# Kernel optimization log

Measured on AMD Instinct MI355X. Metric: run time of the kernel, lower is better.

The kernel has to match this reference:

```python
import jax, jax.numpy as jnp
import numpy as np

EMB, HID, V_SRC, V_TGT, NUM_OUT, BOS = 128, 512, 10000, 8000, 9, 0


def _lstm_cell(x, h, c, Wih, Whh, bih, bhh):
    # PyTorch LSTMCell math: gates ordered i, f, g, o
    g = x @ Wih.T + h @ Whh.T + (bih + bhh)
    i, f, gg, o = jnp.split(g, 4, axis=-1)
    i, f, o = jax.nn.sigmoid(i), jax.nn.sigmoid(f), jax.nn.sigmoid(o)
    c = f * c + i * jnp.tanh(gg)
    h = o * jnp.tanh(c)
    return h, c


def setup_inputs() -> dict:
    key = jax.random.key(0)
    ks = jax.random.split(key, 12)
    s = 1.0 / np.sqrt(HID)
    u = lambda k, shp: jax.random.uniform(k, shp, jnp.float32, -s, s)
    src = jax.random.randint(ks[0], (2048, 2), 0, V_SRC)
    src_embed = jax.random.normal(ks[1], (V_SRC, EMB), jnp.float32)
    src_embed = src_embed.at[0].set(0.0)  # padding_idx row
    tgt_embed = jax.random.normal(ks[2], (V_TGT, EMB), jnp.float32)
    tgt_embed = tgt_embed.at[BOS].set(0.0)  # padding_idx=BOS row
    return {
        "src": src,
        "src_embed": src_embed,
        "tgt_embed": tgt_embed,
        "enc_Wih": u(ks[3], (4 * HID, EMB)),
        "enc_Whh": u(ks[4], (4 * HID, HID)),
        "enc_bih": u(ks[5], (4 * HID,)),
        "enc_bhh": u(ks[6], (4 * HID,)),
        "dec_Wih": u(ks[7], (4 * HID, EMB)),
        "dec_Whh": u(ks[8], (4 * HID, HID)),
        "dec_bih": u(ks[9], (4 * HID,)),
        "dec_bhh": u(ks[10], (4 * HID,)),
        "proj_W": u(ks[11], (V_TGT, HID)),
        "proj_b": jnp.zeros((V_TGT,), jnp.float32),
    }


def reference(src, src_embed, tgt_embed, enc_Wih, enc_Whh, enc_bih, enc_bhh,
              dec_Wih, dec_Whh, dec_bih, dec_bhh, proj_W, proj_b):
    B = src.shape[0]
    # ---- encoder over the 2 source tokens ----
    enc_in = src_embed[src]  # (B, 2, EMB); dropout is identity at inference
    h = jnp.zeros((B, HID), jnp.float32)
    c = jnp.zeros((B, HID), jnp.float32)

    def enc_step(carry, x_t):
        h, c = carry
        h, c = _lstm_cell(x_t, h, c, enc_Wih, enc_Whh, enc_bih, enc_bhh)
        return (h, c), None

    (h, c), _ = jax.lax.scan(enc_step, (h, c), jnp.swapaxes(enc_in, 0, 1))

    token0 = jnp.full((B,), BOS, jnp.int32)

    def dec_step(carry, _):
        token, h, c = carry
        x = tgt_embed[token]  # (B, EMB)
        h, c = _lstm_cell(x, h, c, dec_Wih, dec_Whh, dec_bih, dec_bhh)
        logit = h @ proj_W.T + proj_b  # (B, V_TGT)
        nxt = jnp.argmax(logit, axis=-1).astype(jnp.int32)
        return (nxt, h, c), logit

    _, step_logits = jax.lax.scan(dec_step, (token0, h, c), None, length=NUM_OUT)
    # step_logits: (NUM_OUT, B, V_TGT) -> max-pool over steps
    return jnp.max(step_logits, axis=0)
```

## Files before the change

### kernel.cpp

```cpp
#include <hip/hip_runtime.h>
#include <math.h>

#define BB 2048
#define EMB 128
#define HID 512
#define G4 2048
#define VT 8000
#define VTP2 8192
#define NSTEP 9
#define NTILE2 64
#define LDW 132

typedef short bf16x8 __attribute__((ext_vector_type(8)));
typedef float f32x4 __attribute__((ext_vector_type(4)));

__device__ __forceinline__ ushort f2bf(float x) {
    uint u = __float_as_uint(x);
    uint r = (u + 0x7fffu + ((u >> 16) & 1u)) >> 16;
    return (ushort)r;
}
__device__ __forceinline__ float bf2f(ushort h) {
    return __uint_as_float(((uint)h) << 16);
}
__device__ __forceinline__ float sigm(float x) { return 1.0f / (1.0f + expf(-x)); }

__device__ __forceinline__ void gload16(const ushort* g, ushort* l) {
    __builtin_amdgcn_global_load_lds(
        (const __attribute__((address_space(1))) uint*)g,
        (__attribute__((address_space(3))) uint*)l, 16, 0, 0);
}

__device__ __forceinline__ void stage4(
    ushort* Sb,
    const ushort* __restrict__ Ah, const ushort* __restrict__ Al,
    const ushort* __restrict__ Bh, const ushort* __restrict__ Bl,
    int biA, int biB, int K, int k0, int wid, int lane)
{
    const ushort* src = (wid < 2) ? ((wid == 0) ? Ah : Al)
                                  : ((wid == 2) ? Bh : Bl);
    const int rowbase = (wid < 2) ? biA : biB;
    const int rl = lane >> 2, kcp = lane & 3;
    #pragma unroll
    for (int j = 0; j < 8; ++j) {
        int row = j * 16 + rl;
        int kc = (kcp - (row >> 1)) & 3;
        const ushort* g = src + (size_t)(rowbase + row) * K + k0 + kc * 8;
        gload16(g, Sb + wid * 4096 + j * 512);
    }
}

__device__ __forceinline__ void stage8(
    ushort* Sb,
    const ushort* __restrict__ Ah, const ushort* __restrict__ Al,
    const ushort* __restrict__ Bh, const ushort* __restrict__ Bl,
    int biA, int biB, int K, int k0, int wid, int lane)
{
    const int rl = lane >> 2, kcp = lane & 3;
    #pragma unroll
    for (int j = 0; j < 4; ++j) {
        int c = wid * 4 + j;
        int region = c >> 3;
        int rowblk = c & 7;
        int row = rowblk * 16 + rl;
        int kc = (kcp - (row >> 1)) & 3;
        const ushort* src = (region < 2) ? (region == 0 ? Ah : Al)
                                         : (region == 2 ? Bh : Bl);
        int base = (region < 2) ? biA : biB;
        gload16(src + (size_t)(base + row) * K + k0 + kc * 8,
                Sb + region * 4096 + rowblk * 512);
    }
}

__global__ __launch_bounds__(64) void gather2_kernel(
    ushort* __restrict__ Xhi, ushort* __restrict__ Xlo,
    const float* __restrict__ table,
    const int* __restrict__ src, int mode, int offset,
    const float* __restrict__ partval, const int* __restrict__ partidx)
{
    int row = blockIdx.x, t = threadIdx.x;
    int tok;
    if (mode == 0) {
        tok = src[row * 2 + offset];
    } else if (mode == 1) {
        tok = 0;
    } else {
        float v = partval[(size_t)row * NTILE2 + t];
        int  ix = partidx[(size_t)row * NTILE2 + t];
        #pragma unroll
        for (int off = 1; off < 64; off <<= 1) {
            float ov = __shfl_xor(v, off, 64);
            int   oi = __shfl_xor(ix, off, 64);
            if (ov > v || (ov == v && oi < ix)) { v = ov; ix = oi; }
        }
        tok = ix;
    }
    float2 e = *(const float2*)&table[(size_t)tok * EMB + t * 2];
    ushort2 hh, hl;
    hh.x = f2bf(e.x); hl.x = f2bf(e.x - bf2f(hh.x));
    hh.y = f2bf(e.y); hl.y = f2bf(e.y - bf2f(hh.y));
    *(ushort2*)&Xhi[row * EMB + t * 2] = hh;
    *(ushort2*)&Xlo[row * EMB + t * 2] = hl;
}

__global__ __launch_bounds__(256) void convgate_kernel(
    const float* __restrict__ W, ushort* __restrict__ Whi, ushort* __restrict__ Wlo,
    int kshift)
{
    size_t e0 = ((size_t)blockIdx.x * 256 + threadIdx.x) * 8;
    int K = 1 << kshift;
    int in_row = (int)(e0 >> kshift);
    int q = in_row & 511, gate = in_row >> 9;
    size_t o0 = (((size_t)(q * 4 + gate)) << kshift) + (e0 & (K - 1));
    float4 v0 = *(const float4*)&W[e0];
    float4 v1 = *(const float4*)&W[e0 + 4];
    float x[8] = {v0.x, v0.y, v0.z, v0.w, v1.x, v1.y, v1.z, v1.w};
    uint p[4], qq[4];
    #pragma unroll
    for (int j = 0; j < 4; ++j) {
        ushort h0 = f2bf(x[2 * j]),     l0 = f2bf(x[2 * j] - bf2f(h0));
        ushort h1 = f2bf(x[2 * j + 1]), l1 = f2bf(x[2 * j + 1] - bf2f(h1));
        p[j]  = (uint)h0 | ((uint)h1 << 16);
        qq[j] = (uint)l0 | ((uint)l1 << 16);
    }
    *(uint4*)&Whi[o0] = make_uint4(p[0], p[1], p[2], p[3]);
    *(uint4*)&Wlo[o0] = make_uint4(qq[0], qq[1], qq[2], qq[3]);
}

__global__ __launch_bounds__(256) void convgbias_kernel(
    const float* __restrict__ b0, const float* __restrict__ b1, float* __restrict__ bp)
{
    int i = blockIdx.x * 256 + threadIdx.x;
    int q = i >> 2, gate = i & 3;
    bp[i] = b0[gate * 512 + q] + b1[gate * 512 + q];
}

__global__ __launch_bounds__(256) void convw_kernel(
    const float* __restrict__ W, ushort* __restrict__ Whi, ushort* __restrict__ Wlo)
{
    size_t e0 = ((size_t)blockIdx.x * 256 + threadIdx.x) * 8;
    int row = (int)(e0 >> 9);
    uint p[4], q[4];
    if (row < VT) {
        float4 v0 = *(const float4*)&W[e0];
        float4 v1 = *(const float4*)&W[e0 + 4];
        float x[8] = {v0.x, v0.y, v0.z, v0.w, v1.x, v1.y, v1.z, v1.w};
        #pragma unroll
        for (int j = 0; j < 4; ++j) {
            ushort h0 = f2bf(x[2 * j]),     l0 = f2bf(x[2 * j] - bf2f(h0));
            ushort h1 = f2bf(x[2 * j + 1]), l1 = f2bf(x[2 * j + 1] - bf2f(h1));
            p[j] = (uint)h0 | ((uint)h1 << 16);
            q[j] = (uint)l0 | ((uint)l1 << 16);
        }
    } else {
        #pragma unroll
        for (int j = 0; j < 4; ++j) { p[j] = 0u; q[j] = 0u; }
    }
    *(uint4*)&Whi[e0] = make_uint4(p[0], p[1], p[2], p[3]);
    *(uint4*)&Wlo[e0] = make_uint4(q[0], q[1], q[2], q[3]);
}

__global__ __launch_bounds__(256) void convb_kernel(
    const float* __restrict__ b, float* __restrict__ bp)
{
    int i = blockIdx.x * 256 + threadIdx.x;
    if (i < VTP2) bp[i] = (i < VT) ? b[i] : -1e30f;
}

__global__ __launch_bounds__(512) void gatescell_kernel(
    const ushort* __restrict__ Xhi, const ushort* __restrict__ Xlo,
    const ushort* __restrict__ Hhi, const ushort* __restrict__ Hlo,
    const ushort* __restrict__ WihH, const ushort* __restrict__ WihL,
    const ushort* __restrict__ WhhH, const ushort* __restrict__ WhhL,
    const float* __restrict__ bperm,
    float* __restrict__ Cst,
    ushort* __restrict__ OHhi, ushort* __restrict__ OHlo,
    int nk)
{
    __shared__ __align__(16) char smem[128 * LDW * 4];
    ushort* S0 = (ushort*)smem;

    const int t = threadIdx.x;
    const int n = blockIdx.x;
    const int tile = (n & 7) * 2 + ((n >> 3) & 1);
    const int rb = n >> 4;
    const int bj0 = tile * 128;
    const int bi0 = rb * 128;
    const int il = t & 15;
    const int g  = (t >> 4) & 3;
    const int wid = t >> 6;
    const int lane = t & 63;
    const int wr = wid >> 2;
    const int wc = wid & 3;

    int aofs[4], bofs[2];
    #pragma unroll
    for (int m = 0; m < 4; ++m) {
        int r = wr * 64 + m * 16 + il;
        aofs[m] = r * 32 + (((g + (r >> 1)) & 3) << 3);
    }
    #pragma unroll
    for (int nn = 0; nn < 2; ++nn) {
        int r = wc * 32 + nn * 16 + il;
        bofs[nn] = 8192 + r * 32 + (((g + (r >> 1)) & 3) << 3);
    }

    f32x4 acc[4][2];
    #pragma unroll
    for (int m = 0; m < 4; ++m)
        #pragma unroll
        for (int nn = 0; nn < 2; ++nn) acc[m][nn] = 0.0f;

    stage8(S0, Xhi, Xlo, WihH, WihL, bi0, bj0, EMB, 0, wid, lane);

    for (int ks = 0; ks < nk; ++ks) {
        int cur = ks & 1;
        if (ks + 1 < nk) {
            int kn = ks + 1;
            if (kn < 4) stage8(S0 + (cur ^ 1) * 16384, Xhi, Xlo, WihH, WihL, bi0, bj0, EMB, kn * 32, wid, lane);
            else        stage8(S0 + (cur ^ 1) * 16384, Hhi, Hlo, WhhH, WhhL, bi0, bj0, HID, (kn - 4) * 32, wid, lane);
        }
        if (ks + 1 < nk) asm volatile("s_waitcnt vmcnt(4)" ::: "memory");
        else             asm volatile("s_waitcnt vmcnt(0)" ::: "memory");
        __builtin_amdgcn_s_barrier();
        __builtin_amdgcn_sched_barrier(0);

        ushort* Sb = S0 + cur * 16384;
        bf16x8 ah[4], al[4];
        #pragma unroll
        for (int m = 0; m < 4; ++m) {
            ah[m] = *(const bf16x8*)&Sb[aofs[m]];
            al[m] = *(const bf16x8*)&Sb[4096 + aofs[m]];
        }
        #pragma unroll
        for (int nn = 0; nn < 2; ++nn) {
            bf16x8 bh = *(const bf16x8*)&Sb[bofs[nn]];
            bf16x8 bl = *(const bf16x8*)&Sb[4096 + bofs[nn]];
            #pragma unroll
            for (int m = 0; m < 4; ++m) {
                acc[m][nn] = __builtin_amdgcn_mfma_f32_16x16x32_bf16(ah[m], bh, acc[m][nn], 0, 0, 0);
                acc[m][nn] = __builtin_amdgcn_mfma_f32_16x16x32_bf16(ah[m], bl, acc[m][nn], 0, 0, 0);
                acc[m][nn] = __builtin_amdgcn_mfma_f32_16x16x32_bf16(al[m], bh, acc[m][nn], 0, 0, 0);
            }
        }
        __builtin_amdgcn_sched_barrier(0);
        __builtin_amdgcn_s_barrier();
        __builtin_amdgcn_sched_barrier(0);
    }

    float* Tr = (float*)smem;
    float bn[2];
    #pragma unroll
    for (int nn = 0; nn < 2; ++nn) bn[nn] = bperm[bj0 + wc * 32 + nn * 16 + il];

    #pragma unroll
    for (int m = 0; m < 4; ++m)
        #pragma unroll
        for (int nn = 0; nn < 2; ++nn)
            #pragma unroll
            for (int j = 0; j < 4; ++j)
                Tr[(wr * 64 + m * 16 + g * 4 + j) * LDW + wc * 32 + nn * 16 + il]
                    = acc[m][nn][j] + bn[nn];
    __syncthreads();

    #pragma unroll
    for (int it = 0; it < 8; ++it) {
        int row = it * 16 + (t >> 5);
        int c4 = t & 31;
        float4 gv = *(float4*)&Tr[row * LDW + c4 * 4];
        float gi = sigm(gv.x), gf = sigm(gv.y), gg = tanhf(gv.z), go = sigm(gv.w);
        size_t o = (size_t)(bi0 + row) * HID + (bj0 >> 2) + c4;
        float cnew = gf * Cst[o] + gi * gg;
        float h = go * tanhf(cnew);
        Cst[o] = cnew;
        ushort hh = f2bf(h);
        OHhi[o] = hh;
        OHlo[o] = f2bf(h - bf2f(hh));
    }
}

__global__ __launch_bounds__(256) void proj_kernel(
    const ushort* __restrict__ Ahi, const ushort* __restrict__ Alo,
    const ushort* __restrict__ Whi, const ushort* __restrict__ Wlo,
    const float* __restrict__ biasp,
    float* __restrict__ outmax,
    float* __restrict__ partval, int* __restrict__ partidx,
    int mode)
{
    __shared__ __align__(16) char smem[128 * LDW * 4];
    ushort* S0 = (ushort*)smem;

    const int t = threadIdx.x;
    const int n = blockIdx.x;
    const int xcd = n & 7;
    const int j8 = n >> 3;
    const int tile = xcd * 8 + (j8 & 7);
    const int rb = j8 >> 3;
    const int bj0 = tile * 128;
    const int bi0 = rb * 128;
    const int il = t & 15;
    const int g  = (t >> 4) & 3;
    const int wid = t >> 6;
    const int lane = t & 63;
    const int wr = wid >> 1, wc = wid & 1;

    float4 oldv[16];
    const bool rmw = (mode == 2);
    if (rmw) {
        #pragma unroll
        for (int it = 0; it < 16; ++it) {
            int row2 = it * 8 + (t >> 5);
            oldv[it] = *(const float4*)&outmax[(size_t)(bi0 + row2) * VT + bj0 + (t & 31) * 4];
        }
    }

    int aofs[4], bofs[4];
    #pragma unroll
    for (int m = 0; m < 4; ++m) {
        int r = wr * 64 + m * 16 + il;
        aofs[m] = r * 32 + (((g + (r >> 1)) & 3) << 3);
    }
    #pragma unroll
    for (int nn = 0; nn < 4; ++nn) {
        int r = wc * 64 + nn * 16 + il;
        bofs[nn] = 8192 + r * 32 + (((g + (r >> 1)) & 3) << 3);
    }

    f32x4 acc[4][4];
    #pragma unroll
    for (int m = 0; m < 4; ++m)
        #pragma unroll
        for (int nn = 0; nn < 4; ++nn) acc[m][nn] = 0.0f;

    stage4(S0, Ahi, Alo, Whi, Wlo, bi0, bj0, HID, 0, wid, lane);

    for (int ks = 0; ks < 16; ++ks) {
        int cur = ks & 1;
        if (ks + 1 < 16)
            stage4(S0 + (cur ^ 1) * 16384, Ahi, Alo, Whi, Wlo, bi0, bj0, HID, (ks + 1) * 32, wid, lane);
        if (ks + 1 < 16) asm volatile("s_waitcnt vmcnt(8)" ::: "memory");
        else             asm volatile("s_waitcnt vmcnt(0)" ::: "memory");
        __builtin_amdgcn_s_barrier();
        __builtin_amdgcn_sched_barrier(0);

        ushort* Sb = S0 + cur * 16384;
        bf16x8 ah[4], al[4];
        #pragma unroll
        for (int m = 0; m < 4; ++m) {
            ah[m] = *(const bf16x8*)&Sb[aofs[m]];
            al[m] = *(const bf16x8*)&Sb[4096 + aofs[m]];
        }
        #pragma unroll
        for (int nn = 0; nn < 4; ++nn) {
            bf16x8 bh = *(const bf16x8*)&Sb[bofs[nn]];
            bf16x8 bl = *(const bf16x8*)&Sb[4096 + bofs[nn]];
            #pragma unroll
            for (int m = 0; m < 4; ++m) {
                acc[m][nn] = __builtin_amdgcn_mfma_f32_16x16x32_bf16(ah[m], bh, acc[m][nn], 0, 0, 0);
                acc[m][nn] = __builtin_amdgcn_mfma_f32_16x16x32_bf16(ah[m], bl, acc[m][nn], 0, 0, 0);
                acc[m][nn] = __builtin_amdgcn_mfma_f32_16x16x32_bf16(al[m], bh, acc[m][nn], 0, 0, 0);
            }
        }
        __builtin_amdgcn_sched_barrier(0);
        __builtin_amdgcn_s_barrier();
        __builtin_amdgcn_sched_barrier(0);
    }

    float* Tr = (float*)smem;
    float bn[4];
    #pragma unroll
    for (int nn = 0; nn < 4; ++nn) bn[nn] = biasp[bj0 + wc * 64 + nn * 16 + il];

    #pragma unroll
    for (int m = 0; m < 4; ++m)
        #pragma unroll
        for (int nn = 0; nn < 4; ++nn)
            #pragma unroll
            for (int j = 0; j < 4; ++j)
                Tr[(wr * 64 + m * 16 + g * 4 + j) * LDW + wc * 64 + nn * 16 + il]
                    = acc[m][nn][j] + bn[nn];
    __syncthreads();

    #pragma unroll
    for (int it = 0; it < 16; ++it) {
        int row2 = it * 8 + (t >> 5);
        int c4 = t & 31;
        int row = bi0 + row2;
        int col = bj0 + c4 * 4;
        float4 cur = *(float4*)&Tr[row2 * LDW + c4 * 4];

        float bv = cur.x; int bix = col;
        if (cur.y > bv) { bv = cur.y; bix = col + 1; }
        if (cur.z > bv) { bv = cur.z; bix = col + 2; }
        if (cur.w > bv) { bv = cur.w; bix = col + 3; }
        #pragma unroll
        for (int off = 1; off < 32; off <<= 1) {
            float ov = __shfl_xor(bv, off, 64);
            int   oi = __shfl_xor(bix, off, 64);
            if (ov > bv || (ov == bv && oi < bix)) { bv = ov; bix = oi; }
        }
        if ((t & 31) == 0) {
            partval[(size_t)row * NTILE2 + tile] = bv;
            partidx[(size_t)row * NTILE2 + tile] = bix;
        }

        if (col < VT) {
            float4 o = cur;
            if (rmw) {
                float4 p = oldv[it];
                o.x = fmaxf(o.x, p.x); o.y = fmaxf(o.y, p.y);
                o.z = fmaxf(o.z, p.z); o.w = fmaxf(o.w, p.w);
            }
            *(float4*)&outmax[(size_t)row * VT + col] = o;
        }
    }
}

extern "C" void kernel_launch(void* const* d_in, const int* in_sizes, int n_in,
                              void* d_out, int out_size, void* d_ws, size_t ws_size,
                              hipStream_t stream) {
    const int*   src       = (const int*)d_in[0];
    const float* src_embed = (const float*)d_in[1];
    const float* tgt_embed = (const float*)d_in[2];
    const float* enc_Wih   = (const float*)d_in[3];
    const float* enc_Whh   = (const float*)d_in[4];
    const float* enc_bih   = (const float*)d_in[5];
    const float* enc_bhh   = (const float*)d_in[6];
    const float* dec_Wih   = (const float*)d_in[7];
    const float* dec_Whh   = (const float*)d_in[8];
    const float* dec_bih   = (const float*)d_in[9];
    const float* dec_bhh   = (const float*)d_in[10];
    const float* proj_W    = (const float*)d_in[11];
    const float* proj_b    = (const float*)d_in[12];
    float* out = (float*)d_out;

    char* ws = (char*)d_ws;
    float*  C     = (float*)ws;   ws += (size_t)BB * HID * 4;
    float*  PV    = (float*)ws;   ws += (size_t)BB * NTILE2 * 4;
    int*    PI    = (int*)ws;     ws += (size_t)BB * NTILE2 * 4;
    ushort* Xhi   = (ushort*)ws;  ws += (size_t)BB * EMB * 2;
    ushort* Xlo   = (ushort*)ws;  ws += (size_t)BB * EMB * 2;
    ushort* Hhi   = (ushort*)ws;  ws += (size_t)BB * HID * 2;
    ushort* Hlo   = (ushort*)ws;  ws += (size_t)BB * HID * 2;
    ushort* PWhi  = (ushort*)ws;  ws += (size_t)VTP2 * HID * 2;
    ushort* PWlo  = (ushort*)ws;  ws += (size_t)VTP2 * HID * 2;
    float*  biasp = (float*)ws;   ws += (size_t)VTP2 * 4;
    ushort* eWihH = (ushort*)ws;  ws += (size_t)G4 * EMB * 2;
    ushort* eWihL = (ushort*)ws;  ws += (size_t)G4 * EMB * 2;
    ushort* eWhhH = (ushort*)ws;  ws += (size_t)G4 * HID * 2;
    ushort* eWhhL = (ushort*)ws;  ws += (size_t)G4 * HID * 2;
    ushort* dWihH = (ushort*)ws;  ws += (size_t)G4 * EMB * 2;
    ushort* dWihL = (ushort*)ws;  ws += (size_t)G4 * EMB * 2;
    ushort* dWhhH = (ushort*)ws;  ws += (size_t)G4 * HID * 2;
    ushort* dWhhL = (ushort*)ws;  ws += (size_t)G4 * HID * 2;
    float*  BSe   = (float*)ws;   ws += (size_t)G4 * 4;
    float*  BSd   = (float*)ws;   ws += (size_t)G4 * 4;

    hipMemsetAsync(C, 0, (size_t)BB * HID * 4, stream);

    convw_kernel<<<VTP2 * HID / 8 / 256, 256, 0, stream>>>(proj_W, PWhi, PWlo);
    convb_kernel<<<VTP2 / 256, 256, 0, stream>>>(proj_b, biasp);
    convgate_kernel<<<G4 * EMB / 8 / 256, 256, 0, stream>>>(enc_Wih, eWihH, eWihL, 7);
    convgate_kernel<<<G4 * HID / 8 / 256, 256, 0, stream>>>(enc_Whh, eWhhH, eWhhL, 9);
    convgate_kernel<<<G4 * EMB / 8 / 256, 256, 0, stream>>>(dec_Wih, dWihH, dWihL, 7);
    convgate_kernel<<<G4 * HID / 8 / 256, 256, 0, stream>>>(dec_Whh, dWhhH, dWhhL, 9);
    convgbias_kernel<<<G4 / 256, 256, 0, stream>>>(enc_bih, enc_bhh, BSe);
    convgbias_kernel<<<G4 / 256, 256, 0, stream>>>(dec_bih, dec_bhh, BSd);

    for (int tstep = 0; tstep < 2; ++tstep) {
        gather2_kernel<<<BB, 64, 0, stream>>>(Xhi, Xlo, src_embed, src, 0, tstep, PV, PI);
        gatescell_kernel<<<256, 512, 0, stream>>>(Xhi, Xlo, Hhi, Hlo,
            eWihH, eWihL, eWhhH, eWhhL, BSe, C, Hhi, Hlo, tstep == 0 ? 4 : 20);
    }

    for (int s = 0; s < NSTEP; ++s) {
        gather2_kernel<<<BB, 64, 0, stream>>>(Xhi, Xlo, tgt_embed, nullptr,
            (s == 0 ? 1 : 2), 0, PV, PI);
        gatescell_kernel<<<256, 512, 0, stream>>>(Xhi, Xlo, Hhi, Hlo,
            dWihH, dWihL, dWhhH, dWhhL, BSd, C, Hhi, Hlo, 20);
        proj_kernel<<<1024, 256, 0, stream>>>(Hhi, Hlo, PWhi, PWlo, biasp,
            out, PV, PI, (s == 0 ? 1 : 2));
    }
}
```

Measured before the change: 1.043 ms.

## Enlarge projection tiles to 128x256 with triple-buffered split-phase LDS pipeline

The projection GEMM moves from 128x128 tiles with 256 threads and double buffering to 128x256 tiles with 512 threads. It uses a three-stage LDS ring, and each k-step is split into two halves with interleaved loads and setprio around the MFMA blocks. The epilogue now writes the output and argmax per 16-row chunk through a smaller transpose buffer, reading the old max values inline instead of prefetching them into registers. The per-row partial argmax count drops from 64 to 32 tiles. The goal is more reuse of each staged tile and better overlap of loads with compute, at the cost of 144KB of LDS and one block per CU.

```diff
diff --git a/kernel.cpp b/kernel.cpp
--- a/kernel.cpp
+++ b/kernel.cpp
@@ -8,7 +8,7 @@
 #define VT 8000
 #define VTP2 8192
 #define NSTEP 9
-#define NTILE2 64
+#define PT 32
 #define LDW 132
 
 typedef short bf16x8 __attribute__((ext_vector_type(8)));
@@ -28,25 +28,6 @@
     __builtin_amdgcn_global_load_lds(
         (const __attribute__((address_space(1))) uint*)g,
         (__attribute__((address_space(3))) uint*)l, 16, 0, 0);
-}
-
-__device__ __forceinline__ void stage4(
-    ushort* Sb,
-    const ushort* __restrict__ Ah, const ushort* __restrict__ Al,
-    const ushort* __restrict__ Bh, const ushort* __restrict__ Bl,
-    int biA, int biB, int K, int k0, int wid, int lane)
-{
-    const ushort* src = (wid < 2) ? ((wid == 0) ? Ah : Al)
-                                  : ((wid == 2) ? Bh : Bl);
-    const int rowbase = (wid < 2) ? biA : biB;
-    const int rl = lane >> 2, kcp = lane & 3;
-    #pragma unroll
-    for (int j = 0; j < 8; ++j) {
-        int row = j * 16 + rl;
-        int kc = (kcp - (row >> 1)) & 3;
-        const ushort* g = src + (size_t)(rowbase + row) * K + k0 + kc * 8;
-        gload16(g, Sb + wid * 4096 + j * 512);
-    }
 }
 
 __device__ __forceinline__ void stage8(
@@ -71,6 +52,27 @@
     }
 }
 
+__device__ __forceinline__ void stage3h(
+    ushort* Sb,
+    const ushort* __restrict__ Ah, const ushort* __restrict__ Al,
+    const ushort* __restrict__ Bh, const ushort* __restrict__ Bl,
+    int biA, int biB, int k0, int wid, int lane, int half)
+{
+    const int rl = lane >> 2, kcp = lane & 3;
+    #pragma unroll
+    for (int j = 0; j < 3; ++j) {
+        int c = wid * 6 + half * 3 + j;
+        const ushort* src;
+        int row, base;
+        if (c < 8)       { src = Ah; row = c * 16 + rl;        base = biA; }
+        else if (c < 16) { src = Al; row = (c - 8) * 16 + rl;  base = biA; }
+        else if (c < 32) { src = Bh; row = (c - 16) * 16 + rl; base = biB; }
+        else             { src = Bl; row = (c - 32) * 16 + rl; base = biB; }
+        int kc = (kcp - (row >> 1)) & 3;
+        gload16(src + (size_t)(base + row) * HID + k0 + kc * 8, Sb + c * 512);
+    }
+}
+
 __global__ __launch_bounds__(64) void gather2_kernel(
     ushort* __restrict__ Xhi, ushort* __restrict__ Xlo,
     const float* __restrict__ table,
@@ -84,8 +86,8 @@
     } else if (mode == 1) {
         tok = 0;
     } else {
-        float v = partval[(size_t)row * NTILE2 + t];
-        int  ix = partidx[(size_t)row * NTILE2 + t];
+        float v = (t < PT) ? partval[(size_t)row * PT + t] : -INFINITY;
+        int  ix = (t < PT) ? partidx[(size_t)row * PT + t] : 0x7fffffff;
         #pragma unroll
         for (int off = 1; off < 64; off <<= 1) {
             float ov = __shfl_xor(v, off, 64);
@@ -278,7 +280,7 @@
     }
 }
 
-__global__ __launch_bounds__(256) void proj_kernel(
+__global__ __launch_bounds__(512, 1) void proj_kernel(
     const ushort* __restrict__ Ahi, const ushort* __restrict__ Alo,
     const ushort* __restrict__ Whi, const ushort* __restrict__ Wlo,
     const float* __restrict__ biasp,
@@ -286,32 +288,23 @@
     float* __restrict__ partval, int* __restrict__ partidx,
     int mode)
 {
-    __shared__ __align__(16) char smem[128 * LDW * 4];
+    __shared__ __align__(16) char smem[147456];
     ushort* S0 = (ushort*)smem;
 
     const int t = threadIdx.x;
     const int n = blockIdx.x;
     const int xcd = n & 7;
-    const int j8 = n >> 3;
-    const int tile = xcd * 8 + (j8 & 7);
-    const int rb = j8 >> 3;
-    const int bj0 = tile * 128;
+    const int j6 = n >> 3;
+    const int tile = xcd * 4 + (j6 & 3);
+    const int rb = j6 >> 2;
+    const int bj0 = tile * 256;
     const int bi0 = rb * 128;
     const int il = t & 15;
     const int g  = (t >> 4) & 3;
     const int wid = t >> 6;
     const int lane = t & 63;
-    const int wr = wid >> 1, wc = wid & 1;
-
-    float4 oldv[16];
-    const bool rmw = (mode == 2);
-    if (rmw) {
-        #pragma unroll
-        for (int it = 0; it < 16; ++it) {
-            int row2 = it * 8 + (t >> 5);
-            oldv[it] = *(const float4*)&outmax[(size_t)(bi0 + row2) * VT + bj0 + (t & 31) * 4];
-        }
-    }
+    const int wr = wid >> 2;
+    const int wc = wid & 3;
 
     int aofs[4], bofs[4];
     #pragma unroll
@@ -331,35 +324,73 @@
         #pragma unroll
         for (int nn = 0; nn < 4; ++nn) acc[m][nn] = 0.0f;
 
-    stage4(S0, Ahi, Alo, Whi, Wlo, bi0, bj0, HID, 0, wid, lane);
-
+    stage3h(S0,         Ahi, Alo, Whi, Wlo, bi0, bj0, 0,  wid, lane, 0);
+    stage3h(S0,         Ahi, Alo, Whi, Wlo, bi0, bj0, 0,  wid, lane, 1);
+    stage3h(S0 + 24576, Ahi, Alo, Whi, Wlo, bi0, bj0, 32, wid, lane, 0);
+    stage3h(S0 + 24576, Ahi, Alo, Whi, Wlo, bi0, bj0, 32, wid, lane, 1);
+    asm volatile("s_waitcnt vmcnt(6)" ::: "memory");
+    __builtin_amdgcn_s_barrier();
+    __builtin_amdgcn_sched_barrier(0);
+
+    #pragma unroll 1
     for (int ks = 0; ks < 16; ++ks) {
-        int cur = ks & 1;
-        if (ks + 1 < 16)
-            stage4(S0 + (cur ^ 1) * 16384, Ahi, Alo, Whi, Wlo, bi0, bj0, HID, (ks + 1) * 32, wid, lane);
-        if (ks + 1 < 16) asm volatile("s_waitcnt vmcnt(8)" ::: "memory");
-        else             asm volatile("s_waitcnt vmcnt(0)" ::: "memory");
+        ushort* Sb = S0 + (ks % 3) * 24576;
+        ushort* Sn = S0 + ((ks + 2) % 3) * 24576;
+
+        bf16x8 a0h[2], a0l[2], bh[4], bl[4], a1h[2], a1l[2];
+        #pragma unroll
+        for (int m = 0; m < 2; ++m) {
+            a0h[m] = *(const bf16x8*)&Sb[aofs[m]];
+            a0l[m] = *(const bf16x8*)&Sb[4096 + aofs[m]];
+        }
+        #pragma unroll
+        for (int nn = 0; nn < 4; ++nn) {
+            bh[nn] = *(const bf16x8*)&Sb[bofs[nn]];
+            bl[nn] = *(const bf16x8*)&Sb[8192 + bofs[nn]];
+        }
+        if (ks + 2 < 16)
+            stage3h(Sn, Ahi, Alo, Whi, Wlo, bi0, bj0, (ks + 2) * 32, wid, lane, 0);
         __builtin_amdgcn_s_barrier();
         __builtin_amdgcn_sched_barrier(0);
-
-        ushort* Sb = S0 + cur * 16384;
-        bf16x8 ah[4], al[4];
-        #pragma unroll
-        for (int m = 0; m < 4; ++m) {
-            ah[m] = *(const bf16x8*)&Sb[aofs[m]];
-            al[m] = *(const bf16x8*)&Sb[4096 + aofs[m]];
-        }
-        #pragma unroll
-        for (int nn = 0; nn < 4; ++nn) {
-            bf16x8 bh = *(const bf16x8*)&Sb[bofs[nn]];
-            bf16x8 bl = *(const bf16x8*)&Sb[4096 + bofs[nn]];
+        asm volatile("s_waitcnt lgkmcnt(0)" ::: "memory");
+        __builtin_amdgcn_sched_barrier(0);
+        __builtin_amdgcn_s_setprio(1);
+        #pragma unroll
+        for (int nn = 0; nn < 4; ++nn)
             #pragma unroll
-            for (int m = 0; m < 4; ++m) {
-                acc[m][nn] = __builtin_amdgcn_mfma_f32_16x16x32_bf16(ah[m], bh, acc[m][nn], 0, 0, 0);
-                acc[m][nn] = __builtin_amdgcn_mfma_f32_16x16x32_bf16(ah[m], bl, acc[m][nn], 0, 0, 0);
-                acc[m][nn] = __builtin_amdgcn_mfma_f32_16x16x32_bf16(al[m], bh, acc[m][nn], 0, 0, 0);
+            for (int m = 0; m < 2; ++m) {
+                acc[m][nn] = __builtin_amdgcn_mfma_f32_16x16x32_bf16(a0h[m], bh[nn], acc[m][nn], 0, 0, 0);
+                acc[m][nn] = __builtin_amdgcn_mfma_f32_16x16x32_bf16(a0h[m], bl[nn], acc[m][nn], 0, 0, 0);
+                acc[m][nn] = __builtin_amdgcn_mfma_f32_16x16x32_bf16(a0l[m], bh[nn], acc[m][nn], 0, 0, 0);
             }
-        }
+        __builtin_amdgcn_s_setprio(0);
+        __builtin_amdgcn_sched_barrier(0);
+        __builtin_amdgcn_s_barrier();
+        __builtin_amdgcn_sched_barrier(0);
+
+        #pragma unroll
+        for (int m = 0; m < 2; ++m) {
+            a1h[m] = *(const bf16x8*)&Sb[aofs[2 + m]];
+            a1l[m] = *(const bf16x8*)&Sb[4096 + aofs[2 + m]];
+        }
+        if (ks + 2 < 16)
+            stage3h(Sn, Ahi, Alo, Whi, Wlo, bi0, bj0, (ks + 2) * 32, wid, lane, 1);
+        if (ks + 2 < 16)      asm volatile("s_waitcnt vmcnt(6)" ::: "memory");
+        else if (ks + 1 < 16) asm volatile("s_waitcnt vmcnt(0)" ::: "memory");
+        __builtin_amdgcn_s_barrier();
+        __builtin_amdgcn_sched_barrier(0);
+        asm volatile("s_waitcnt lgkmcnt(0)" ::: "memory");
+        __builtin_amdgcn_sched_barrier(0);
+        __builtin_amdgcn_s_setprio(1);
+        #pragma unroll
+        for (int nn = 0; nn < 4; ++nn)
+            #pragma unroll
+            for (int m = 0; m < 2; ++m) {
+                acc[2 + m][nn] = __builtin_amdgcn_mfma_f32_16x16x32_bf16(a1h[m], bh[nn], acc[2 + m][nn], 0, 0, 0);
+                acc[2 + m][nn] = __builtin_amdgcn_mfma_f32_16x16x32_bf16(a1h[m], bl[nn], acc[2 + m][nn], 0, 0, 0);
+                acc[2 + m][nn] = __builtin_amdgcn_mfma_f32_16x16x32_bf16(a1l[m], bh[nn], acc[2 + m][nn], 0, 0, 0);
+            }
+        __builtin_amdgcn_s_setprio(0);
         __builtin_amdgcn_sched_barrier(0);
         __builtin_amdgcn_s_barrier();
         __builtin_amdgcn_sched_barrier(0);
@@ -371,47 +402,48 @@
     for (int nn = 0; nn < 4; ++nn) bn[nn] = biasp[bj0 + wc * 64 + nn * 16 + il];
 
     #pragma unroll
-    for (int m = 0; m < 4; ++m)
+    for (int m = 0; m < 4; ++m) {
         #pragma unroll
         for (int nn = 0; nn < 4; ++nn)
             #pragma unroll
             for (int j = 0; j < 4; ++j)
-                Tr[(wr * 64 + m * 16 + g * 4 + j) * LDW + wc * 64 + nn * 16 + il]
-                    = acc[m][nn][j] + bn[nn];
-    __syncthreads();
-
-    #pragma unroll
-    for (int it = 0; it < 16; ++it) {
-        int row2 = it * 8 + (t >> 5);
-        int c4 = t & 31;
-        int row = bi0 + row2;
-        int col = bj0 + c4 * 4;
-        float4 cur = *(float4*)&Tr[row2 * LDW + c4 * 4];
-
-        float bv = cur.x; int bix = col;
-        if (cur.y > bv) { bv = cur.y; bix = col + 1; }
-        if (cur.z > bv) { bv = cur.z; bix = col + 2; }
-        if (cur.w > bv) { bv = cur.w; bix = col + 3; }
-        #pragma unroll
-        for (int off = 1; off < 32; off <<= 1) {
-            float ov = __shfl_xor(bv, off, 64);
-            int   oi = __shfl_xor(bix, off, 64);
-            if (ov > bv || (ov == bv && oi < bix)) { bv = ov; bix = oi; }
-        }
-        if ((t & 31) == 0) {
-            partval[(size_t)row * NTILE2 + tile] = bv;
-            partidx[(size_t)row * NTILE2 + tile] = bix;
-        }
-
-        if (col < VT) {
-            float4 o = cur;
-            if (rmw) {
-                float4 p = oldv[it];
-                o.x = fmaxf(o.x, p.x); o.y = fmaxf(o.y, p.y);
-                o.z = fmaxf(o.z, p.z); o.w = fmaxf(o.w, p.w);
+                Tr[(wr * 16 + g * 4 + j) * 260 + wc * 64 + nn * 16 + il] = acc[m][nn][j] + bn[nn];
+        __syncthreads();
+        #pragma unroll
+        for (int it = 0; it < 4; ++it) {
+            int lr2 = it * 8 + wid;
+            int c0 = lane * 4;
+            int row = bi0 + m * 16 + ((lr2 >> 4) << 6) + (lr2 & 15);
+            int col = bj0 + c0;
+            float4 cur = *(float4*)&Tr[lr2 * 260 + c0];
+
+            float bv = cur.x; int bix = col;
+            if (cur.y > bv) { bv = cur.y; bix = col + 1; }
+            if (cur.z > bv) { bv = cur.z; bix = col + 2; }
+            if (cur.w > bv) { bv = cur.w; bix = col + 3; }
+            #pragma unroll
+            for (int off = 1; off < 64; off <<= 1) {
+                float ov = __shfl_xor(bv, off, 64);
+                int   oi = __shfl_xor(bix, off, 64);
+                if (ov > bv || (ov == bv && oi < bix)) { bv = ov; bix = oi; }
             }
-            *(float4*)&outmax[(size_t)row * VT + col] = o;
-        }
+            if (lane == 0) {
+                partval[(size_t)row * PT + tile] = bv;
+                partidx[(size_t)row * PT + tile] = bix;
+            }
+
+            if (col < VT) {
+                float* op = &outmax[(size_t)row * VT + col];
+                float4 o = cur;
+                if (mode == 2) {
+                    float4 p = *(const float4*)op;
+                    o.x = fmaxf(o.x, p.x); o.y = fmaxf(o.y, p.y);
+                    o.z = fmaxf(o.z, p.z); o.w = fmaxf(o.w, p.w);
+                }
+                *(float4*)op = o;
+            }
+        }
+        __syncthreads();
     }
 }
 
@@ -435,8 +467,8 @@
 
     char* ws = (char*)d_ws;
     float*  C     = (float*)ws;   ws += (size_t)BB * HID * 4;
-    float*  PV    = (float*)ws;   ws += (size_t)BB * NTILE2 * 4;
-    int*    PI    = (int*)ws;     ws += (size_t)BB * NTILE2 * 4;
+    float*  PV    = (float*)ws;   ws += (size_t)BB * 64 * 4;
+    int*    PI    = (int*)ws;     ws += (size_t)BB * 64 * 4;
     ushort* Xhi   = (ushort*)ws;  ws += (size_t)BB * EMB * 2;
     ushort* Xlo   = (ushort*)ws;  ws += (size_t)BB * EMB * 2;
     ushort* Hhi   = (ushort*)ws;  ws += (size_t)BB * HID * 2;
@@ -477,7 +509,7 @@
             (s == 0 ? 1 : 2), 0, PV, PI);
         gatescell_kernel<<<256, 512, 0, stream>>>(Xhi, Xlo, Hhi, Hlo,
             dWihH, dWihL, dWhhH, dWhhL, BSd, C, Hhi, Hlo, 20);
-        proj_kernel<<<1024, 256, 0, stream>>>(Hhi, Hlo, PWhi, PWlo, biasp,
+        proj_kernel<<<512, 512, 0, stream>>>(Hhi, Hlo, PWhi, PWlo, biasp,
             out, PV, PI, (s == 0 ? 1 : 2));
     }
 }
```

After: 1.046 ms. About the same (+0.3%).

## Shrink projection kernel LDS and registers by splitting hi/lo passes and chunked epilogue

Applied to the files above, without the earlier changes.

The projection GEMM now stages only one A and one B operand per K-step and walks the three hi/lo product combinations as 48 sequential K-groups, which halves the LDS buffer. The epilogue transposes and reduces 16 rows at a time instead of the whole 128-row tile. The register-held prefetch of the old output values is removed and replaced by loads inside the epilogue. Together these lower LDS and register pressure so more blocks can be resident per CU. The cost is three times as many barrier-separated K iterations, operands reloaded from global memory for each pass, and extra syncs in the epilogue.

```diff
diff --git a/kernel.cpp b/kernel.cpp
--- a/kernel.cpp
+++ b/kernel.cpp
@@ -30,22 +30,19 @@
         (__attribute__((address_space(3))) uint*)l, 16, 0, 0);
 }
 
-__device__ __forceinline__ void stage4(
-    ushort* Sb,
-    const ushort* __restrict__ Ah, const ushort* __restrict__ Al,
-    const ushort* __restrict__ Bh, const ushort* __restrict__ Bl,
-    int biA, int biB, int K, int k0, int wid, int lane)
-{
-    const ushort* src = (wid < 2) ? ((wid == 0) ? Ah : Al)
-                                  : ((wid == 2) ? Bh : Bl);
-    const int rowbase = (wid < 2) ? biA : biB;
+__device__ __forceinline__ void stage2(
+    ushort* Sb, const ushort* __restrict__ A, const ushort* __restrict__ B,
+    int biA, int biB, int k0, int wid, int lane)
+{
     const int rl = lane >> 2, kcp = lane & 3;
     #pragma unroll
-    for (int j = 0; j < 8; ++j) {
-        int row = j * 16 + rl;
+    for (int j = 0; j < 4; ++j) {
+        int c = wid * 4 + j;
+        const ushort* src = (c < 8) ? A : B;
+        int base = (c < 8) ? biA : biB;
+        int row = (c & 7) * 16 + rl;
         int kc = (kcp - (row >> 1)) & 3;
-        const ushort* g = src + (size_t)(rowbase + row) * K + k0 + kc * 8;
-        gload16(g, Sb + wid * 4096 + j * 512);
+        gload16(src + (size_t)(base + row) * HID + k0 + kc * 8, Sb + c * 512);
     }
 }
 
@@ -286,7 +283,7 @@
     float* __restrict__ partval, int* __restrict__ partidx,
     int mode)
 {
-    __shared__ __align__(16) char smem[128 * LDW * 4];
+    __shared__ __align__(16) char smem[32768];
     ushort* S0 = (ushort*)smem;
 
     const int t = threadIdx.x;
@@ -303,16 +300,6 @@
     const int lane = t & 63;
     const int wr = wid >> 1, wc = wid & 1;
 
-    float4 oldv[16];
-    const bool rmw = (mode == 2);
-    if (rmw) {
-        #pragma unroll
-        for (int it = 0; it < 16; ++it) {
-            int row2 = it * 8 + (t >> 5);
-            oldv[it] = *(const float4*)&outmax[(size_t)(bi0 + row2) * VT + bj0 + (t & 31) * 4];
-        }
-    }
-
     int aofs[4], bofs[4];
     #pragma unroll
     for (int m = 0; m < 4; ++m) {
@@ -322,7 +309,7 @@
     #pragma unroll
     for (int nn = 0; nn < 4; ++nn) {
         int r = wc * 64 + nn * 16 + il;
-        bofs[nn] = 8192 + r * 32 + (((g + (r >> 1)) & 3) << 3);
+        bofs[nn] = 4096 + r * 32 + (((g + (r >> 1)) & 3) << 3);
     }
 
     f32x4 acc[4][4];
@@ -331,35 +318,35 @@
         #pragma unroll
         for (int nn = 0; nn < 4; ++nn) acc[m][nn] = 0.0f;
 
-    stage4(S0, Ahi, Alo, Whi, Wlo, bi0, bj0, HID, 0, wid, lane);
-
-    for (int ks = 0; ks < 16; ++ks) {
-        int cur = ks & 1;
-        if (ks + 1 < 16)
-            stage4(S0 + (cur ^ 1) * 16384, Ahi, Alo, Whi, Wlo, bi0, bj0, HID, (ks + 1) * 32, wid, lane);
-        if (ks + 1 < 16) asm volatile("s_waitcnt vmcnt(8)" ::: "memory");
+    const ushort* PA[3] = {Ahi, Ahi, Alo};
+    const ushort* PB[3] = {Whi, Wlo, Whi};
+
+    stage2(S0, PA[0], PB[0], bi0, bj0, 0, wid, lane);
+
+    #pragma unroll 1
+    for (int kg = 0; kg < 48; ++kg) {
+        int cur = kg & 1;
+        if (kg + 1 < 48) {
+            int kn = kg + 1;
+            stage2(S0 + (cur ^ 1) * 8192, PA[kn >> 4], PB[kn >> 4],
+                   bi0, bj0, (kn & 15) * 32, wid, lane);
+        }
+        if (kg + 1 < 48) asm volatile("s_waitcnt vmcnt(4)" ::: "memory");
         else             asm volatile("s_waitcnt vmcnt(0)" ::: "memory");
         __builtin_amdgcn_s_barrier();
         __builtin_amdgcn_sched_barrier(0);
 
-        ushort* Sb = S0 + cur * 16384;
-        bf16x8 ah[4], al[4];
-        #pragma unroll
-        for (int m = 0; m < 4; ++m) {
-            ah[m] = *(const bf16x8*)&Sb[aofs[m]];
-            al[m] = *(const bf16x8*)&Sb[4096 + aofs[m]];
-        }
-        #pragma unroll
-        for (int nn = 0; nn < 4; ++nn) {
-            bf16x8 bh = *(const bf16x8*)&Sb[bofs[nn]];
-            bf16x8 bl = *(const bf16x8*)&Sb[4096 + bofs[nn]];
+        ushort* Sb = S0 + cur * 8192;
+        bf16x8 ah[4], bh[4];
+        #pragma unroll
+        for (int m = 0; m < 4; ++m) ah[m] = *(const bf16x8*)&Sb[aofs[m]];
+        #pragma unroll
+        for (int nn = 0; nn < 4; ++nn) bh[nn] = *(const bf16x8*)&Sb[bofs[nn]];
+        #pragma unroll
+        for (int nn = 0; nn < 4; ++nn)
             #pragma unroll
-            for (int m = 0; m < 4; ++m) {
-                acc[m][nn] = __builtin_amdgcn_mfma_f32_16x16x32_bf16(ah[m], bh, acc[m][nn], 0, 0, 0);
-                acc[m][nn] = __builtin_amdgcn_mfma_f32_16x16x32_bf16(ah[m], bl, acc[m][nn], 0, 0, 0);
-                acc[m][nn] = __builtin_amdgcn_mfma_f32_16x16x32_bf16(al[m], bh, acc[m][nn], 0, 0, 0);
-            }
-        }
+            for (int m = 0; m < 4; ++m)
+                acc[m][nn] = __builtin_amdgcn_mfma_f32_16x16x32_bf16(ah[m], bh[nn], acc[m][nn], 0, 0, 0);
         __builtin_amdgcn_sched_barrier(0);
         __builtin_amdgcn_s_barrier();
         __builtin_amdgcn_sched_barrier(0);
@@ -371,47 +358,48 @@
     for (int nn = 0; nn < 4; ++nn) bn[nn] = biasp[bj0 + wc * 64 + nn * 16 + il];
 
     #pragma unroll
-    for (int m = 0; m < 4; ++m)
+    for (int m = 0; m < 4; ++m) {
         #pragma unroll
         for (int nn = 0; nn < 4; ++nn)
             #pragma unroll
             for (int j = 0; j < 4; ++j)
-                Tr[(wr * 64 + m * 16 + g * 4 + j) * LDW + wc * 64 + nn * 16 + il]
-                    = acc[m][nn][j] + bn[nn];
-    __syncthreads();
-
-    #pragma unroll
-    for (int it = 0; it < 16; ++it) {
-        int row2 = it * 8 + (t >> 5);
-        int c4 = t & 31;
-        int row = bi0 + row2;
-        int col = bj0 + c4 * 4;
-        float4 cur = *(float4*)&Tr[row2 * LDW + c4 * 4];
-
-        float bv = cur.x; int bix = col;
-        if (cur.y > bv) { bv = cur.y; bix = col + 1; }
-        if (cur.z > bv) { bv = cur.z; bix = col + 2; }
-        if (cur.w > bv) { bv = cur.w; bix = col + 3; }
-        #pragma unroll
-        for (int off = 1; off < 32; off <<= 1) {
-            float ov = __shfl_xor(bv, off, 64);
-            int   oi = __shfl_xor(bix, off, 64);
-            if (ov > bv || (ov == bv && oi < bix)) { bv = ov; bix = oi; }
-        }
-        if ((t & 31) == 0) {
-            partval[(size_t)row * NTILE2 + tile] = bv;
-            partidx[(size_t)row * NTILE2 + tile] = bix;
-        }
-
-        if (col < VT) {
-            float4 o = cur;
-            if (rmw) {
-                float4 p = oldv[it];
-                o.x = fmaxf(o.x, p.x); o.y = fmaxf(o.y, p.y);
-                o.z = fmaxf(o.z, p.z); o.w = fmaxf(o.w, p.w);
+                Tr[(wr * 16 + g * 4 + j) * LDW + wc * 64 + nn * 16 + il] = acc[m][nn][j] + bn[nn];
+        __syncthreads();
+        #pragma unroll
+        for (int it = 0; it < 4; ++it) {
+            int lr2 = it * 8 + (t >> 5);
+            int c4 = t & 31;
+            int row = bi0 + m * 16 + ((lr2 >> 4) << 6) + (lr2 & 15);
+            int col = bj0 + c4 * 4;
+            float4 cur = *(float4*)&Tr[lr2 * LDW + c4 * 4];
+
+            float bv = cur.x; int bix = col;
+            if (cur.y > bv) { bv = cur.y; bix = col + 1; }
+            if (cur.z > bv) { bv = cur.z; bix = col + 2; }
+            if (cur.w > bv) { bv = cur.w; bix = col + 3; }
+            #pragma unroll
+            for (int off = 1; off < 32; off <<= 1) {
+                float ov = __shfl_xor(bv, off, 64);
+                int   oi = __shfl_xor(bix, off, 64);
+                if (ov > bv || (ov == bv && oi < bix)) { bv = ov; bix = oi; }
             }
-            *(float4*)&outmax[(size_t)row * VT + col] = o;
-        }
+            if ((t & 31) == 0) {
+                partval[(size_t)row * NTILE2 + tile] = bv;
+                partidx[(size_t)row * NTILE2 + tile] = bix;
+            }
+
+            if (col < VT) {
+                float* op = &outmax[(size_t)row * VT + col];
+                float4 o = cur;
+                if (mode == 2) {
+                    float4 p = *(const float4*)op;
+                    o.x = fmaxf(o.x, p.x); o.y = fmaxf(o.y, p.y);
+                    o.z = fmaxf(o.z, p.z); o.w = fmaxf(o.w, p.w);
+                }
+                *(float4*)op = o;
+            }
+        }
+        __syncthreads();
     }
 }
 
```

Measured after the change: 1.140 ms. 1.09x slower.
